# Optimization experiments

Measured on AMD Instinct MI355X. Metric: run time of the kernel, lower is better.

## Reference

```python
import jax, jax.numpy as jnp
import numpy as np

B = 16384          # batch
N = 24             # num_features / fields
CARD = 10000       # vocab per feature (all equal)
D = 16             # factor_dim
NI = N * (N - 1) // 2  # 276 pairwise interactions
H1, H2 = 128, 64


def setup_inputs() -> dict:
    key = jax.random.key(0)
    ks = jax.random.split(key, 10)
    x = jax.random.randint(ks[0], (B, N), 0, CARD, dtype=jnp.int32)
    # field-aware embedding table: E[f, id, field, :] is feature f's embedding w.r.t. field
    E = jax.random.normal(ks[1], (N, CARD, N, D), dtype=jnp.float32) * 0.01
    Wlin = jax.random.normal(ks[2], (N, CARD), dtype=jnp.float32) * 0.01
    blin = jnp.zeros((1,), dtype=jnp.float32)
    W1 = jax.random.normal(ks[3], (NI, H1), dtype=jnp.float32) * (1.0 / np.sqrt(NI))
    b1 = jnp.zeros((H1,), dtype=jnp.float32)
    W2 = jax.random.normal(ks[4], (H1, H2), dtype=jnp.float32) * (1.0 / np.sqrt(H1))
    b2 = jnp.zeros((H2,), dtype=jnp.float32)
    W3 = jax.random.normal(ks[5], (H2, 1), dtype=jnp.float32) * (1.0 / np.sqrt(H2))
    b3 = jnp.zeros((1,), dtype=jnp.float32)
    return {"x": x, "E": E, "Wlin": Wlin, "blin": blin,
            "W1": W1, "b1": b1, "W2": W2, "b2": b2, "W3": W3, "b3": b3}


def reference(x, E, Wlin, blin, W1, b1, W2, b2, W3, b3):
    feat_idx = jnp.arange(N)[None, :]              # [1, N]
    # factors[b, i, j, :] = embedding of feature i (value x[b,i]) w.r.t. field j
    factors = E[feat_idx, x]                        # [B, N, N, D]
    # interactions[b, i, j] = <factors[b,i,j], factors[b,j,i]>
    inter = jnp.sum(factors * jnp.swapaxes(factors, 1, 2), axis=-1)  # [B, N, N]
    iu, ju = jnp.triu_indices(N, k=1)
    pairs = inter[:, iu, ju]                        # [B, NI] strict upper triangle, row-major
    # FCN (dropout inactive at inference): relu -> relu -> linear
    h = jax.nn.relu(pairs @ W1 + b1)
    h = jax.nn.relu(h @ W2 + b2)
    nn_out = h @ W3 + b3                            # [B, 1]
    lin_out = jnp.sum(Wlin[feat_idx, x], axis=1, keepdims=True) + blin  # [B, 1]
    return lin_out + nn_out
```

## Files before the change

kernel.cpp:

```cpp
#include <hip/hip_runtime.h>

#define BB    16384
#define NF    24
#define CARDN 10000
#define DD    16
#define NI    276
#define H1N   128
#define H2N   64
#define SB    16
#define PSTR  17
#define HSTR  17

__global__ __launch_bounds__(256, 4) void fanfm_fused_kernel(
    const int* __restrict__ x, const float* __restrict__ E,
    const float* __restrict__ Wlin, const float* __restrict__ blin,
    const float* __restrict__ W1, const float* __restrict__ b1,
    const float* __restrict__ W2, const float* __restrict__ b2,
    const float* __restrict__ W3, const float* __restrict__ b3,
    float* __restrict__ out)
{
    __shared__ float pairsT[NI * PSTR];
    __shared__ float h1T[H1N * HSTR];
    __shared__ int   xs[SB * NF];
    __shared__ float lin_s[SB];
    __shared__ int   pi_tab[NI];
    __shared__ int   pj_tab[NI];

    float* h2T = pairsT;

    const int tid = threadIdx.x;
    const int b0  = blockIdx.x * SB;

    for (int idx = tid; idx < SB * NF; idx += 256) xs[idx] = x[b0 * NF + idx];
    for (int idx = tid; idx < NI; idx += 256) {
        int i = 0, rem = idx, cnt = NF - 1;
        while (rem >= cnt) { rem -= cnt; --cnt; ++i; }
        pi_tab[idx] = i;
        pj_tab[idx] = i + 1 + rem;
    }
    __syncthreads();

    if (tid < SB) {
        float l = blin[0] + b3[0];
        #pragma unroll
        for (int i = 0; i < NF; ++i) l += Wlin[i * CARDN + xs[tid * NF + i]];
        lin_s[tid] = l;
    }

    #pragma unroll 2
    for (int k = 0; k < (SB * NI + 255) / 256; ++k) {
        int idx = tid + k * 256;
        if (idx < SB * NI) {
            int s = idx / NI;
            int p = idx - s * NI;
            int i = pi_tab[p];
            int j = pj_tab[p];
            int xi = xs[s * NF + i];
            int xj = xs[s * NF + j];
            const float4* a = (const float4*)(E + ((size_t)i * CARDN + xi) * (NF * DD) + j * DD);
            const float4* c = (const float4*)(E + ((size_t)j * CARDN + xj) * (NF * DD) + i * DD);
            float4 a0 = a[0], a1 = a[1], a2 = a[2], a3 = a[3];
            float4 c0 = c[0], c1 = c[1], c2 = c[2], c3 = c[3];
            float d =
                a0.x*c0.x + a0.y*c0.y + a0.z*c0.z + a0.w*c0.w +
                a1.x*c1.x + a1.y*c1.y + a1.z*c1.z + a1.w*c1.w +
                a2.x*c2.x + a2.y*c2.y + a2.z*c2.z + a2.w*c2.w +
                a3.x*c3.x + a3.y*c3.y + a3.z*c3.z + a3.w*c3.w;
            pairsT[p * PSTR + s] = d;
        }
    }
    __syncthreads();

    {
        const int c4 = tid & 31;
        const int sg = tid >> 5;
        float acc[2][4] = {};
        #pragma unroll 4
        for (int p = 0; p < NI; ++p) {
            float4 w = *(const float4*)(W1 + p * H1N + c4 * 4);
            float pr0 = pairsT[p * PSTR + sg * 2 + 0];
            float pr1 = pairsT[p * PSTR + sg * 2 + 1];
            acc[0][0] = fmaf(pr0, w.x, acc[0][0]);
            acc[0][1] = fmaf(pr0, w.y, acc[0][1]);
            acc[0][2] = fmaf(pr0, w.z, acc[0][2]);
            acc[0][3] = fmaf(pr0, w.w, acc[0][3]);
            acc[1][0] = fmaf(pr1, w.x, acc[1][0]);
            acc[1][1] = fmaf(pr1, w.y, acc[1][1]);
            acc[1][2] = fmaf(pr1, w.z, acc[1][2]);
            acc[1][3] = fmaf(pr1, w.w, acc[1][3]);
        }
        float4 bb = *(const float4*)(b1 + c4 * 4);
        #pragma unroll
        for (int si = 0; si < 2; ++si) {
            int s = sg * 2 + si;
            h1T[(c4 * 4 + 0) * HSTR + s] = fmaxf(acc[si][0] + bb.x, 0.f);
            h1T[(c4 * 4 + 1) * HSTR + s] = fmaxf(acc[si][1] + bb.y, 0.f);
            h1T[(c4 * 4 + 2) * HSTR + s] = fmaxf(acc[si][2] + bb.z, 0.f);
            h1T[(c4 * 4 + 3) * HSTR + s] = fmaxf(acc[si][3] + bb.w, 0.f);
        }
    }
    __syncthreads();

    {
        const int c16 = tid & 15;
        const int sg2 = tid >> 4;
        float acc[4] = {};
        #pragma unroll 4
        for (int p = 0; p < H1N; ++p) {
            float4 w = *(const float4*)(W2 + p * H2N + c16 * 4);
            float pr = h1T[p * HSTR + sg2];
            acc[0] = fmaf(pr, w.x, acc[0]);
            acc[1] = fmaf(pr, w.y, acc[1]);
            acc[2] = fmaf(pr, w.z, acc[2]);
            acc[3] = fmaf(pr, w.w, acc[3]);
        }
        float4 bb = *(const float4*)(b2 + c16 * 4);
        h2T[(c16 * 4 + 0) * HSTR + sg2] = fmaxf(acc[0] + bb.x, 0.f);
        h2T[(c16 * 4 + 1) * HSTR + sg2] = fmaxf(acc[1] + bb.y, 0.f);
        h2T[(c16 * 4 + 2) * HSTR + sg2] = fmaxf(acc[2] + bb.z, 0.f);
        h2T[(c16 * 4 + 3) * HSTR + sg2] = fmaxf(acc[3] + bb.w, 0.f);
    }
    __syncthreads();

    {
        const int s  = tid >> 4;
        const int ko = tid & 15;
        float r = 0.f;
        #pragma unroll
        for (int kk = 0; kk < 4; ++kk) {
            int k = ko * 4 + kk;
            r = fmaf(h2T[k * HSTR + s], W3[k], r);
        }
        r += __shfl_xor(r, 1);
        r += __shfl_xor(r, 2);
        r += __shfl_xor(r, 4);
        r += __shfl_xor(r, 8);
        if (ko == 0) out[b0 + s] = r + lin_s[s];
    }
}

extern "C" void kernel_launch(void* const* d_in, const int* in_sizes, int n_in,
                              void* d_out, int out_size, void* d_ws, size_t ws_size,
                              hipStream_t stream) {
    const int*   x    = (const int*)  d_in[0];
    const float* E    = (const float*)d_in[1];
    const float* Wlin = (const float*)d_in[2];
    const float* blin = (const float*)d_in[3];
    const float* W1   = (const float*)d_in[4];
    const float* b1   = (const float*)d_in[5];
    const float* W2   = (const float*)d_in[6];
    const float* b2   = (const float*)d_in[7];
    const float* W3   = (const float*)d_in[8];
    const float* b3   = (const float*)d_in[9];
    float* out = (float*)d_out;

    fanfm_fused_kernel<<<BB / SB, 256, 0, stream>>>(
        x, E, Wlin, blin, W1, b1, W2, b2, W3, b3, out);
}
```

Baseline: 133.5 us.

## Specialize waves into embedding-gather producers and an MLP consumer wave

Halves samples per block to 8 and doubles the block to 512 threads. 448 threads gather the field-aware embeddings and compute the pairwise dot products. One 64-thread wave computes the linear term, then spins on an LDS atomic counter and runs all three MLP layers in registers, with a shuffle reduction at the end. This removes several block-wide barriers and the h2 staging buffer, and aims to overlap one block's MLP with other blocks' memory-bound gathers. In exchange a single wave does the whole MLP per block, and the tighter launch bound may limit registers.

```diff
diff --git a/kernel.cpp b/kernel.cpp
--- a/kernel.cpp
+++ b/kernel.cpp
@@ -7,11 +7,13 @@
 #define NI    276
 #define H1N   128
 #define H2N   64
-#define SB    16
-#define PSTR  17
-#define HSTR  17
+#define SB    8
+#define PSTR  9
+#define HSTR  9
+#define NPROD 448
+#define NPAIR (SB * NI)
 
-__global__ __launch_bounds__(256, 4) void fanfm_fused_kernel(
+__global__ __launch_bounds__(512, 8) void fanfm_pc_kernel(
     const int* __restrict__ x, const float* __restrict__ E,
     const float* __restrict__ Wlin, const float* __restrict__ blin,
     const float* __restrict__ W1, const float* __restrict__ b1,
@@ -22,120 +24,118 @@
     __shared__ float pairsT[NI * PSTR];
     __shared__ float h1T[H1N * HSTR];
     __shared__ int   xs[SB * NF];
-    __shared__ float lin_s[SB];
     __shared__ int   pi_tab[NI];
     __shared__ int   pj_tab[NI];
-
-    float* h2T = pairsT;
+    __shared__ int   done;
 
     const int tid = threadIdx.x;
     const int b0  = blockIdx.x * SB;
 
-    for (int idx = tid; idx < SB * NF; idx += 256) xs[idx] = x[b0 * NF + idx];
-    for (int idx = tid; idx < NI; idx += 256) {
-        int i = 0, rem = idx, cnt = NF - 1;
+    if (tid == 0) done = 0;
+    for (int idx = tid; idx < SB * NF; idx += 512) xs[idx] = x[b0 * NF + idx];
+    if (tid < NI) {
+        int i = 0, rem = tid, cnt = NF - 1;
         while (rem >= cnt) { rem -= cnt; --cnt; ++i; }
-        pi_tab[idx] = i;
-        pj_tab[idx] = i + 1 + rem;
+        pi_tab[tid] = i;
+        pj_tab[tid] = i + 1 + rem;
     }
     __syncthreads();
 
-    if (tid < SB) {
-        float l = blin[0] + b3[0];
+    if (tid < NPROD) {
+        #pragma unroll 2
+        for (int k = 0; k < 5; ++k) {
+            int idx = tid + k * NPROD;
+            if (idx < NPAIR) {
+                int s = idx / NI;
+                int p = idx - s * NI;
+                int i = pi_tab[p];
+                int j = pj_tab[p];
+                int xi = xs[s * NF + i];
+                int xj = xs[s * NF + j];
+                const float4* a = (const float4*)(E + ((size_t)i * CARDN + xi) * (NF * DD) + j * DD);
+                const float4* c = (const float4*)(E + ((size_t)j * CARDN + xj) * (NF * DD) + i * DD);
+                float4 a0 = a[0], a1 = a[1], a2 = a[2], a3 = a[3];
+                float4 c0 = c[0], c1 = c[1], c2 = c[2], c3 = c[3];
+                float d =
+                    a0.x*c0.x + a0.y*c0.y + a0.z*c0.z + a0.w*c0.w +
+                    a1.x*c1.x + a1.y*c1.y + a1.z*c1.z + a1.w*c1.w +
+                    a2.x*c2.x + a2.y*c2.y + a2.z*c2.z + a2.w*c2.w +
+                    a3.x*c3.x + a3.y*c3.y + a3.z*c3.z + a3.w*c3.w;
+                pairsT[p * PSTR + s] = d;
+            }
+        }
+        __threadfence_block();
+        atomicAdd(&done, 1);
+    } else {
+        const int ct = tid - NPROD;
+        const int s  = ct >> 3;
+        const int cg = ct & 7;
+
+        float lpart = 0.f;
         #pragma unroll
-        for (int i = 0; i < NF; ++i) l += Wlin[i * CARDN + xs[tid * NF + i]];
-        lin_s[tid] = l;
-    }
+        for (int f = cg * 3; f < cg * 3 + 3; ++f)
+            lpart += Wlin[f * CARDN + xs[s * NF + f]];
 
-    #pragma unroll 2
-    for (int k = 0; k < (SB * NI + 255) / 256; ++k) {
-        int idx = tid + k * 256;
-        if (idx < SB * NI) {
-            int s = idx / NI;
-            int p = idx - s * NI;
-            int i = pi_tab[p];
-            int j = pj_tab[p];
-            int xi = xs[s * NF + i];
-            int xj = xs[s * NF + j];
-            const float4* a = (const float4*)(E + ((size_t)i * CARDN + xi) * (NF * DD) + j * DD);
-            const float4* c = (const float4*)(E + ((size_t)j * CARDN + xj) * (NF * DD) + i * DD);
-            float4 a0 = a[0], a1 = a[1], a2 = a[2], a3 = a[3];
-            float4 c0 = c[0], c1 = c[1], c2 = c[2], c3 = c[3];
-            float d =
-                a0.x*c0.x + a0.y*c0.y + a0.z*c0.z + a0.w*c0.w +
-                a1.x*c1.x + a1.y*c1.y + a1.z*c1.z + a1.w*c1.w +
-                a2.x*c2.x + a2.y*c2.y + a2.z*c2.z + a2.w*c2.w +
-                a3.x*c3.x + a3.y*c3.y + a3.z*c3.z + a3.w*c3.w;
-            pairsT[p * PSTR + s] = d;
+        while (atomicAdd(&done, 0) < NPROD) __builtin_amdgcn_s_sleep(2);
+
+        float acc[16];
+        #pragma unroll
+        for (int c = 0; c < 16; ++c) acc[c] = 0.f;
+        for (int p = 0; p < NI; ++p) {
+            float pr = pairsT[p * PSTR + s];
+            const float4* wr = (const float4*)(W1 + p * H1N + cg * 16);
+            float4 w0 = wr[0], w1 = wr[1], w2 = wr[2], w3 = wr[3];
+            acc[0]  = fmaf(pr, w0.x, acc[0]);  acc[1]  = fmaf(pr, w0.y, acc[1]);
+            acc[2]  = fmaf(pr, w0.z, acc[2]);  acc[3]  = fmaf(pr, w0.w, acc[3]);
+            acc[4]  = fmaf(pr, w1.x, acc[4]);  acc[5]  = fmaf(pr, w1.y, acc[5]);
+            acc[6]  = fmaf(pr, w1.z, acc[6]);  acc[7]  = fmaf(pr, w1.w, acc[7]);
+            acc[8]  = fmaf(pr, w2.x, acc[8]);  acc[9]  = fmaf(pr, w2.y, acc[9]);
+            acc[10] = fmaf(pr, w2.z, acc[10]); acc[11] = fmaf(pr, w2.w, acc[11]);
+            acc[12] = fmaf(pr, w3.x, acc[12]); acc[13] = fmaf(pr, w3.y, acc[13]);
+            acc[14] = fmaf(pr, w3.z, acc[14]); acc[15] = fmaf(pr, w3.w, acc[15]);
         }
-    }
-    __syncthreads();
+        {
+            const float4* br = (const float4*)(b1 + cg * 16);
+            float4 bb0 = br[0], bb1 = br[1], bb2 = br[2], bb3 = br[3];
+            const float bbv[16] = {bb0.x,bb0.y,bb0.z,bb0.w, bb1.x,bb1.y,bb1.z,bb1.w,
+                                   bb2.x,bb2.y,bb2.z,bb2.w, bb3.x,bb3.y,bb3.z,bb3.w};
+            #pragma unroll
+            for (int c = 0; c < 16; ++c)
+                h1T[(cg * 16 + c) * HSTR + s] = fmaxf(acc[c] + bbv[c], 0.f);
+        }
 
-    {
-        const int c4 = tid & 31;
-        const int sg = tid >> 5;
-        float acc[2][4] = {};
-        #pragma unroll 4
-        for (int p = 0; p < NI; ++p) {
-            float4 w = *(const float4*)(W1 + p * H1N + c4 * 4);
-            float pr0 = pairsT[p * PSTR + sg * 2 + 0];
-            float pr1 = pairsT[p * PSTR + sg * 2 + 1];
-            acc[0][0] = fmaf(pr0, w.x, acc[0][0]);
-            acc[0][1] = fmaf(pr0, w.y, acc[0][1]);
-            acc[0][2] = fmaf(pr0, w.z, acc[0][2]);
-            acc[0][3] = fmaf(pr0, w.w, acc[0][3]);
-            acc[1][0] = fmaf(pr1, w.x, acc[1][0]);
-            acc[1][1] = fmaf(pr1, w.y, acc[1][1]);
-            acc[1][2] = fmaf(pr1, w.z, acc[1][2]);
-            acc[1][3] = fmaf(pr1, w.w, acc[1][3]);
+        float acc2[8];
+        #pragma unroll
+        for (int c = 0; c < 8; ++c) acc2[c] = 0.f;
+        for (int p = 0; p < H1N; ++p) {
+            float pr = h1T[p * HSTR + s];
+            const float4* wr = (const float4*)(W2 + p * H2N + cg * 8);
+            float4 w0 = wr[0], w1 = wr[1];
+            acc2[0] = fmaf(pr, w0.x, acc2[0]); acc2[1] = fmaf(pr, w0.y, acc2[1]);
+            acc2[2] = fmaf(pr, w0.z, acc2[2]); acc2[3] = fmaf(pr, w0.w, acc2[3]);
+            acc2[4] = fmaf(pr, w1.x, acc2[4]); acc2[5] = fmaf(pr, w1.y, acc2[5]);
+            acc2[6] = fmaf(pr, w1.z, acc2[6]); acc2[7] = fmaf(pr, w1.w, acc2[7]);
         }
-        float4 bb = *(const float4*)(b1 + c4 * 4);
-        #pragma unroll
-        for (int si = 0; si < 2; ++si) {
-            int s = sg * 2 + si;
-            h1T[(c4 * 4 + 0) * HSTR + s] = fmaxf(acc[si][0] + bb.x, 0.f);
-            h1T[(c4 * 4 + 1) * HSTR + s] = fmaxf(acc[si][1] + bb.y, 0.f);
-            h1T[(c4 * 4 + 2) * HSTR + s] = fmaxf(acc[si][2] + bb.z, 0.f);
-            h1T[(c4 * 4 + 3) * HSTR + s] = fmaxf(acc[si][3] + bb.w, 0.f);
-        }
-    }
-    __syncthreads();
 
-    {
-        const int c16 = tid & 15;
-        const int sg2 = tid >> 4;
-        float acc[4] = {};
-        #pragma unroll 4
-        for (int p = 0; p < H1N; ++p) {
-            float4 w = *(const float4*)(W2 + p * H2N + c16 * 4);
-            float pr = h1T[p * HSTR + sg2];
-            acc[0] = fmaf(pr, w.x, acc[0]);
-            acc[1] = fmaf(pr, w.y, acc[1]);
-            acc[2] = fmaf(pr, w.z, acc[2]);
-            acc[3] = fmaf(pr, w.w, acc[3]);
-        }
-        float4 bb = *(const float4*)(b2 + c16 * 4);
-        h2T[(c16 * 4 + 0) * HSTR + sg2] = fmaxf(acc[0] + bb.x, 0.f);
-        h2T[(c16 * 4 + 1) * HSTR + sg2] = fmaxf(acc[1] + bb.y, 0.f);
-        h2T[(c16 * 4 + 2) * HSTR + sg2] = fmaxf(acc[2] + bb.z, 0.f);
-        h2T[(c16 * 4 + 3) * HSTR + sg2] = fmaxf(acc[3] + bb.w, 0.f);
-    }
-    __syncthreads();
-
-    {
-        const int s  = tid >> 4;
-        const int ko = tid & 15;
-        float r = 0.f;
-        #pragma unroll
-        for (int kk = 0; kk < 4; ++kk) {
-            int k = ko * 4 + kk;
-            r = fmaf(h2T[k * HSTR + s], W3[k], r);
+        float r = lpart;
+        {
+            const float4* br = (const float4*)(b2 + cg * 8);
+            const float4* wr = (const float4*)(W3 + cg * 8);
+            float4 bb0 = br[0], bb1 = br[1];
+            float4 w30 = wr[0], w31 = wr[1];
+            r += fmaxf(acc2[0] + bb0.x, 0.f) * w30.x;
+            r += fmaxf(acc2[1] + bb0.y, 0.f) * w30.y;
+            r += fmaxf(acc2[2] + bb0.z, 0.f) * w30.z;
+            r += fmaxf(acc2[3] + bb0.w, 0.f) * w30.w;
+            r += fmaxf(acc2[4] + bb1.x, 0.f) * w31.x;
+            r += fmaxf(acc2[5] + bb1.y, 0.f) * w31.y;
+            r += fmaxf(acc2[6] + bb1.z, 0.f) * w31.z;
+            r += fmaxf(acc2[7] + bb1.w, 0.f) * w31.w;
         }
         r += __shfl_xor(r, 1);
         r += __shfl_xor(r, 2);
         r += __shfl_xor(r, 4);
-        r += __shfl_xor(r, 8);
-        if (ko == 0) out[b0 + s] = r + lin_s[s];
+        if (cg == 0) out[b0 + s] = r + blin[0] + b3[0];
     }
 }
 
@@ -154,6 +154,6 @@
     const float* b3   = (const float*)d_in[9];
     float* out = (float*)d_out;
 
-    fanfm_fused_kernel<<<BB / SB, 256, 0, stream>>>(
+    fanfm_pc_kernel<<<BB / SB, 512, 0, stream>>>(
         x, E, Wlin, blin, W1, b1, W2, b2, W3, b3, out);
 }
```

Result: slower. 236.8 us (+77.3%).

## Pipeline embedding row gathers into LDS with triple-buffered async loads

Applied to the files above, without the earlier changes.

Replaces per-thread scattered float4 gathers of embedding slices with async global_load_lds copies of each sample's 12-feature row group (all field slices of each feature) into a triple-buffered LDS ring. Dot products for pairs are computed from LDS one stage behind the loads, ordered by a pair table sorted by segment. The per-block sample count drops from 16 to 4, giving 4x more blocks, with 2 blocks per CU, and the MLP layers are remapped to 64 columns by 4 samples, with the second and third layers fused through a wave-wide shuffle reduction. The intent is to overlap gather latency with compute and coalesce the row reads, at the cost of more LDS, lower occupancy and a barrier every stage.

```diff
diff --git a/kernel.cpp b/kernel.cpp
--- a/kernel.cpp
+++ b/kernel.cpp
@@ -7,11 +7,22 @@
 #define NI    276
 #define H1N   128
 #define H2N   64
-#define SB    16
-#define PSTR  17
-#define HSTR  17
+#define SB    4
+#define PSTR  5
+#define GRP   12
+#define ROWF  368
+#define GF    (GRP * ROWF)
+#define F4PG  1104
 
-__global__ __launch_bounds__(256, 4) void fanfm_fused_kernel(
+
+__device__ __forceinline__ void gll16(const float* g, float* l) {
+    __builtin_amdgcn_global_load_lds(
+        (const __attribute__((address_space(1))) unsigned int*)(g),
+        (__attribute__((address_space(3))) unsigned int*)(l),
+        16, 0, 0);
+}
+
+__global__ __launch_bounds__(256, 2) void fanfm_pipe_kernel(
     const int* __restrict__ x, const float* __restrict__ E,
     const float* __restrict__ Wlin, const float* __restrict__ blin,
     const float* __restrict__ W1, const float* __restrict__ b1,
@@ -19,123 +30,116 @@
     const float* __restrict__ W3, const float* __restrict__ b3,
     float* __restrict__ out)
 {
+    __shared__ float buf[3 * GF];
     __shared__ float pairsT[NI * PSTR];
-    __shared__ float h1T[H1N * HSTR];
+    __shared__ float h1T[H1N * PSTR];
     __shared__ int   xs[SB * NF];
+    __shared__ int   ptab[NI];
     __shared__ float lin_s[SB];
-    __shared__ int   pi_tab[NI];
-    __shared__ int   pj_tab[NI];
-
-    float* h2T = pairsT;
+    __shared__ int   cnt01[2];
 
     const int tid = threadIdx.x;
     const int b0  = blockIdx.x * SB;
+    const int wb  = tid & ~63;
 
-    for (int idx = tid; idx < SB * NF; idx += 256) xs[idx] = x[b0 * NF + idx];
-    for (int idx = tid; idx < NI; idx += 256) {
-        int i = 0, rem = idx, cnt = NF - 1;
+    if (tid < SB * NF) xs[tid] = x[b0 * NF + tid];
+    if (tid < 2) cnt01[tid] = (tid == 0) ? 0 : 66;
+    __syncthreads();
+
+    for (int pp = tid; pp < NI; pp += 256) {
+        int i = 0, rem = pp, cnt = NF - 1;
         while (rem >= cnt) { rem -= cnt; --cnt; ++i; }
-        pi_tab[idx] = i;
-        pj_tab[idx] = i + 1 + rem;
+        int j = i + 1 + rem;
+        int seg = (j < GRP) ? 0 : 1;
+        int slot = atomicAdd(&cnt01[seg], 1);
+        ptab[slot] = i | (j << 5) | (pp << 10);
     }
     __syncthreads();
 
     if (tid < SB) {
         float l = blin[0] + b3[0];
         #pragma unroll
-        for (int i = 0; i < NF; ++i) l += Wlin[i * CARDN + xs[tid * NF + i]];
+        for (int f = 0; f < NF; ++f) l += Wlin[f * CARDN + xs[tid * NF + f]];
         lin_s[tid] = l;
     }
 
-    #pragma unroll 2
-    for (int k = 0; k < (SB * NI + 255) / 256; ++k) {
-        int idx = tid + k * 256;
-        if (idx < SB * NI) {
-            int s = idx / NI;
-            int p = idx - s * NI;
-            int i = pi_tab[p];
-            int j = pj_tab[p];
-            int xi = xs[s * NF + i];
-            int xj = xs[s * NF + j];
-            const float4* a = (const float4*)(E + ((size_t)i * CARDN + xi) * (NF * DD) + j * DD);
-            const float4* c = (const float4*)(E + ((size_t)j * CARDN + xj) * (NF * DD) + i * DD);
-            float4 a0 = a[0], a1 = a[1], a2 = a[2], a3 = a[3];
-            float4 c0 = c[0], c1 = c[1], c2 = c[2], c3 = c[3];
-            float d =
-                a0.x*c0.x + a0.y*c0.y + a0.z*c0.z + a0.w*c0.w +
-                a1.x*c1.x + a1.y*c1.y + a1.z*c1.z + a1.w*c1.w +
-                a2.x*c2.x + a2.y*c2.y + a2.z*c2.z + a2.w*c2.w +
-                a3.x*c3.x + a3.y*c3.y + a3.z*c3.z + a3.w*c3.w;
-            pairsT[p * PSTR + s] = d;
+    for (int t = 0; t <= 2 * SB; ++t) {
+        if (t < 2 * SB) {
+            const int g = t & 1;
+            const int s = t >> 1;
+            float* bt = buf + (t % 3) * GF;
+            #pragma unroll
+            for (int k = 0; k < 5; ++k) {
+                int idx = k * 256 + tid;
+                if (idx < F4PG) {
+                    int r   = idx / 92;
+                    int f4i = idx - r * 92;
+                    int c   = f4i >> 2;
+                    int q   = f4i & 3;
+                    int rg  = g * GRP + r;
+                    int j   = c + (c >= rg ? 1 : 0);
+                    const float* src = E
+                        + ((size_t)rg * CARDN + xs[s * NF + rg]) * (NF * DD)
+                        + j * DD + q * 4;
+                    gll16(src, bt + (k * 256 + wb) * 4);
+                }
+            }
         }
+        if (t >= 1) {
+            int segb, segn, s, bA, bB;
+            if (t & 1) { s = t >> 1;       segb = 0;  segn = 66;
+                         bA = (t - 1) % 3; bB = bA; }
+            else       { s = (t >> 1) - 1; segb = 66; segn = 210;
+                         bA = (t - 2) % 3; bB = (t - 1) % 3; }
+            if (tid < segn) {
+                int e = ptab[segb + tid];
+                int i = e & 31, j = (e >> 5) & 31, p = e >> 10;
+                const float4* ra = (const float4*)(buf
+                    + (i < GRP ? bA : bB) * GF + (i % GRP) * ROWF + (j - 1) * DD);
+                const float4* rc = (const float4*)(buf
+                    + (j < GRP ? bA : bB) * GF + (j % GRP) * ROWF + i * DD);
+                float4 a0 = ra[0], a1 = ra[1], a2 = ra[2], a3 = ra[3];
+                float4 c0 = rc[0], c1 = rc[1], c2 = rc[2], c3 = rc[3];
+                float d =
+                    a0.x*c0.x + a0.y*c0.y + a0.z*c0.z + a0.w*c0.w +
+                    a1.x*c1.x + a1.y*c1.y + a1.z*c1.z + a1.w*c1.w +
+                    a2.x*c2.x + a2.y*c2.y + a2.z*c2.z + a2.w*c2.w +
+                    a3.x*c3.x + a3.y*c3.y + a3.z*c3.z + a3.w*c3.w;
+                pairsT[p * PSTR + s] = d;
+            }
+        }
+        __syncthreads();
+    }
+
+    const int c2 = tid & 63;
+    const int sM = tid >> 6;
+    {
+        float a0 = 0.f, a1 = 0.f;
+        #pragma unroll 4
+        for (int p = 0; p < NI; ++p) {
+            float pr = pairsT[p * PSTR + sM];
+            float2 w = *(const float2*)(W1 + p * H1N + c2 * 2);
+            a0 = fmaf(pr, w.x, a0);
+            a1 = fmaf(pr, w.y, a1);
+        }
+        h1T[(c2 * 2 + 0) * PSTR + sM] = fmaxf(a0 + b1[c2 * 2 + 0], 0.f);
+        h1T[(c2 * 2 + 1) * PSTR + sM] = fmaxf(a1 + b1[c2 * 2 + 1], 0.f);
     }
     __syncthreads();
 
     {
-        const int c4 = tid & 31;
-        const int sg = tid >> 5;
-        float acc[2][4] = {};
+        float acc = 0.f;
         #pragma unroll 4
-        for (int p = 0; p < NI; ++p) {
-            float4 w = *(const float4*)(W1 + p * H1N + c4 * 4);
-            float pr0 = pairsT[p * PSTR + sg * 2 + 0];
-            float pr1 = pairsT[p * PSTR + sg * 2 + 1];
-            acc[0][0] = fmaf(pr0, w.x, acc[0][0]);
-            acc[0][1] = fmaf(pr0, w.y, acc[0][1]);
-            acc[0][2] = fmaf(pr0, w.z, acc[0][2]);
-            acc[0][3] = fmaf(pr0, w.w, acc[0][3]);
-            acc[1][0] = fmaf(pr1, w.x, acc[1][0]);
-            acc[1][1] = fmaf(pr1, w.y, acc[1][1]);
-            acc[1][2] = fmaf(pr1, w.z, acc[1][2]);
-            acc[1][3] = fmaf(pr1, w.w, acc[1][3]);
-        }
-        float4 bb = *(const float4*)(b1 + c4 * 4);
-        #pragma unroll
-        for (int si = 0; si < 2; ++si) {
-            int s = sg * 2 + si;
-            h1T[(c4 * 4 + 0) * HSTR + s] = fmaxf(acc[si][0] + bb.x, 0.f);
-            h1T[(c4 * 4 + 1) * HSTR + s] = fmaxf(acc[si][1] + bb.y, 0.f);
-            h1T[(c4 * 4 + 2) * HSTR + s] = fmaxf(acc[si][2] + bb.z, 0.f);
-            h1T[(c4 * 4 + 3) * HSTR + s] = fmaxf(acc[si][3] + bb.w, 0.f);
-        }
-    }
-    __syncthreads();
-
-    {
-        const int c16 = tid & 15;
-        const int sg2 = tid >> 4;
-        float acc[4] = {};
-        #pragma unroll 4
-        for (int p = 0; p < H1N; ++p) {
-            float4 w = *(const float4*)(W2 + p * H2N + c16 * 4);
-            float pr = h1T[p * HSTR + sg2];
-            acc[0] = fmaf(pr, w.x, acc[0]);
-            acc[1] = fmaf(pr, w.y, acc[1]);
-            acc[2] = fmaf(pr, w.z, acc[2]);
-            acc[3] = fmaf(pr, w.w, acc[3]);
-        }
-        float4 bb = *(const float4*)(b2 + c16 * 4);
-        h2T[(c16 * 4 + 0) * HSTR + sg2] = fmaxf(acc[0] + bb.x, 0.f);
-        h2T[(c16 * 4 + 1) * HSTR + sg2] = fmaxf(acc[1] + bb.y, 0.f);
-        h2T[(c16 * 4 + 2) * HSTR + sg2] = fmaxf(acc[2] + bb.z, 0.f);
-        h2T[(c16 * 4 + 3) * HSTR + sg2] = fmaxf(acc[3] + bb.w, 0.f);
-    }
-    __syncthreads();
-
-    {
-        const int s  = tid >> 4;
-        const int ko = tid & 15;
-        float r = 0.f;
-        #pragma unroll
-        for (int kk = 0; kk < 4; ++kk) {
-            int k = ko * 4 + kk;
-            r = fmaf(h2T[k * HSTR + s], W3[k], r);
-        }
+        for (int p = 0; p < H1N; ++p)
+            acc = fmaf(h1T[p * PSTR + sM], W2[p * H2N + c2], acc);
+        float r = fmaxf(acc + b2[c2], 0.f) * W3[c2];
         r += __shfl_xor(r, 1);
         r += __shfl_xor(r, 2);
         r += __shfl_xor(r, 4);
         r += __shfl_xor(r, 8);
-        if (ko == 0) out[b0 + s] = r + lin_s[s];
+        r += __shfl_xor(r, 16);
+        r += __shfl_xor(r, 32);
+        if (c2 == 0) out[b0 + sM] = r + lin_s[sM];
     }
 }
 
@@ -153,7 +157,8 @@
     const float* W3   = (const float*)d_in[8];
     const float* b3   = (const float*)d_in[9];
     float* out = (float*)d_out;
+    (void)d_ws; (void)ws_size; (void)in_sizes; (void)n_in; (void)out_size;
 
-    fanfm_fused_kernel<<<BB / SB, 256, 0, stream>>>(
+    fanfm_pipe_kernel<<<BB / SB, 256, 0, stream>>>(
         x, E, Wlin, blin, W1, b1, W2, b2, W3, b3, out);
 }
```

Result: slower. 320.2 us (+139.8%).

## Stage full embedding rows in LDS with double-buffered per-sample gathers

Applied to the files above, without the earlier changes.

Each sample's 24 field-aware embedding rows are loaded contiguously into a double-buffered shared-memory tile. The next sample's rows are prefetched while pairwise dot products for the current sample are computed from LDS. The second and third MLP layers are also fused into a single reduction. This targets scattered 64-byte global gathers, but it uses about 120 KB of LDS per block and needs a sync each sample, which limits the CU to one block.

```diff
diff --git a/kernel.cpp b/kernel.cpp
--- a/kernel.cpp
+++ b/kernel.cpp
@@ -1,17 +1,20 @@
 #include <hip/hip_runtime.h>
 
-#define BB    16384
-#define NF    24
-#define CARDN 10000
-#define DD    16
-#define NI    276
-#define H1N   128
-#define H2N   64
-#define SB    16
-#define PSTR  17
-#define HSTR  17
+#define BB     16384
+#define NF     24
+#define CARDN  10000
+#define DD     16
+#define NI     276
+#define H1N    128
+#define H2N    64
+#define SB     16
+#define NT     576
+#define CH_F4  5
+#define ROW_F4 121
+#define BUF_F4 (NF * ROW_F4)
+#define PSTR   17
 
-__global__ __launch_bounds__(256, 4) void fanfm_fused_kernel(
+__global__ __launch_bounds__(NT, 1) void fanfm_r8_kernel(
     const int* __restrict__ x, const float* __restrict__ E,
     const float* __restrict__ Wlin, const float* __restrict__ blin,
     const float* __restrict__ W1, const float* __restrict__ b1,
@@ -19,123 +22,122 @@
     const float* __restrict__ W3, const float* __restrict__ b3,
     float* __restrict__ out)
 {
-    __shared__ float pairsT[NI * PSTR];
-    __shared__ float h1T[H1N * HSTR];
-    __shared__ int   xs[SB * NF];
-    __shared__ float lin_s[SB];
-    __shared__ int   pi_tab[NI];
-    __shared__ int   pj_tab[NI];
-
-    float* h2T = pairsT;
+    __shared__ float4 buf[2 * BUF_F4];
+    __shared__ float  pairsT[NI * PSTR];
+    __shared__ float  h1T[H1N * PSTR];
+    __shared__ int    xs[SB * NF];
+    __shared__ float  lin_s[SB];
 
     const int tid = threadIdx.x;
     const int b0  = blockIdx.x * SB;
 
-    for (int idx = tid; idx < SB * NF; idx += 256) xs[idx] = x[b0 * NF + idx];
-    for (int idx = tid; idx < NI; idx += 256) {
-        int i = 0, rem = idx, cnt = NF - 1;
-        while (rem >= cnt) { rem -= cnt; --cnt; ++i; }
-        pi_tab[idx] = i;
-        pj_tab[idx] = i + 1 + rem;
-    }
+    if (tid < SB * NF) xs[tid] = x[b0 * NF + tid];
     __syncthreads();
 
     if (tid < SB) {
         float l = blin[0] + b3[0];
         #pragma unroll
-        for (int i = 0; i < NF; ++i) l += Wlin[i * CARDN + xs[tid * NF + i]];
+        for (int f = 0; f < NF; ++f) l += Wlin[f * CARDN + xs[tid * NF + f]];
         lin_s[tid] = l;
     }
 
-    #pragma unroll 2
-    for (int k = 0; k < (SB * NI + 255) / 256; ++k) {
-        int idx = tid + k * 256;
-        if (idx < SB * NI) {
-            int s = idx / NI;
-            int p = idx - s * NI;
-            int i = pi_tab[p];
-            int j = pj_tab[p];
-            int xi = xs[s * NF + i];
-            int xj = xs[s * NF + j];
-            const float4* a = (const float4*)(E + ((size_t)i * CARDN + xi) * (NF * DD) + j * DD);
-            const float4* c = (const float4*)(E + ((size_t)j * CARDN + xj) * (NF * DD) + i * DD);
-            float4 a0 = a[0], a1 = a[1], a2 = a[2], a3 = a[3];
-            float4 c0 = c[0], c1 = c[1], c2 = c[2], c3 = c[3];
+    int pi = 0, pj = 0;
+    if (tid < NI) {
+        int rem = tid, cnt = NF - 1;
+        while (rem >= cnt) { rem -= cnt; --cnt; ++pi; }
+        pj = pi + 1 + rem;
+    }
+
+    float4 st[4];
+
+    #pragma unroll
+    for (int k = 0; k < 4; ++k) {
+        int v = tid + k * NT;
+        int r = v / 96, w = v - r * 96;
+        st[k] = *((const float4*)(E + ((size_t)r * CARDN + xs[r]) * (NF * DD)) + w);
+    }
+    #pragma unroll
+    for (int k = 0; k < 4; ++k) {
+        int v = tid + k * NT;
+        int r = v / 96, w = v - r * 96;
+        int c = w >> 2, q = w & 3;
+        buf[r * ROW_F4 + c * CH_F4 + q] = st[k];
+    }
+    __syncthreads();
+
+    for (int t = 0; t < SB; ++t) {
+        if (t + 1 < SB) {
+            #pragma unroll
+            for (int k = 0; k < 4; ++k) {
+                int v = tid + k * NT;
+                int r = v / 96, w = v - r * 96;
+                st[k] = *((const float4*)(E +
+                    ((size_t)r * CARDN + xs[(t + 1) * NF + r]) * (NF * DD)) + w);
+            }
+        }
+        if (tid < NI) {
+            const float4* A = &buf[(t & 1) * BUF_F4 + pi * ROW_F4 + pj * CH_F4];
+            const float4* C = &buf[(t & 1) * BUF_F4 + pj * ROW_F4 + pi * CH_F4];
+            float4 a0 = A[0], a1 = A[1], a2 = A[2], a3 = A[3];
+            float4 c0 = C[0], c1 = C[1], c2 = C[2], c3 = C[3];
             float d =
                 a0.x*c0.x + a0.y*c0.y + a0.z*c0.z + a0.w*c0.w +
                 a1.x*c1.x + a1.y*c1.y + a1.z*c1.z + a1.w*c1.w +
                 a2.x*c2.x + a2.y*c2.y + a2.z*c2.z + a2.w*c2.w +
                 a3.x*c3.x + a3.y*c3.y + a3.z*c3.z + a3.w*c3.w;
-            pairsT[p * PSTR + s] = d;
+            pairsT[tid * PSTR + t] = d;
         }
+        if (t + 1 < SB) {
+            #pragma unroll
+            for (int k = 0; k < 4; ++k) {
+                int v = tid + k * NT;
+                int r = v / 96, w = v - r * 96;
+                int c = w >> 2, q = w & 3;
+                buf[((t + 1) & 1) * BUF_F4 + r * ROW_F4 + c * CH_F4 + q] = st[k];
+            }
+        }
+        __syncthreads();
     }
-    __syncthreads();
 
-    {
+    if (tid < 512) {
         const int c4 = tid & 31;
-        const int sg = tid >> 5;
-        float acc[2][4] = {};
+        const int s  = tid >> 5;
+        float acc[4] = {};
         #pragma unroll 4
         for (int p = 0; p < NI; ++p) {
+            float pr = pairsT[p * PSTR + s];
             float4 w = *(const float4*)(W1 + p * H1N + c4 * 4);
-            float pr0 = pairsT[p * PSTR + sg * 2 + 0];
-            float pr1 = pairsT[p * PSTR + sg * 2 + 1];
-            acc[0][0] = fmaf(pr0, w.x, acc[0][0]);
-            acc[0][1] = fmaf(pr0, w.y, acc[0][1]);
-            acc[0][2] = fmaf(pr0, w.z, acc[0][2]);
-            acc[0][3] = fmaf(pr0, w.w, acc[0][3]);
-            acc[1][0] = fmaf(pr1, w.x, acc[1][0]);
-            acc[1][1] = fmaf(pr1, w.y, acc[1][1]);
-            acc[1][2] = fmaf(pr1, w.z, acc[1][2]);
-            acc[1][3] = fmaf(pr1, w.w, acc[1][3]);
-        }
-        float4 bb = *(const float4*)(b1 + c4 * 4);
-        #pragma unroll
-        for (int si = 0; si < 2; ++si) {
-            int s = sg * 2 + si;
-            h1T[(c4 * 4 + 0) * HSTR + s] = fmaxf(acc[si][0] + bb.x, 0.f);
-            h1T[(c4 * 4 + 1) * HSTR + s] = fmaxf(acc[si][1] + bb.y, 0.f);
-            h1T[(c4 * 4 + 2) * HSTR + s] = fmaxf(acc[si][2] + bb.z, 0.f);
-            h1T[(c4 * 4 + 3) * HSTR + s] = fmaxf(acc[si][3] + bb.w, 0.f);
-        }
-    }
-    __syncthreads();
-
-    {
-        const int c16 = tid & 15;
-        const int sg2 = tid >> 4;
-        float acc[4] = {};
-        #pragma unroll 4
-        for (int p = 0; p < H1N; ++p) {
-            float4 w = *(const float4*)(W2 + p * H2N + c16 * 4);
-            float pr = h1T[p * HSTR + sg2];
             acc[0] = fmaf(pr, w.x, acc[0]);
             acc[1] = fmaf(pr, w.y, acc[1]);
             acc[2] = fmaf(pr, w.z, acc[2]);
             acc[3] = fmaf(pr, w.w, acc[3]);
         }
-        float4 bb = *(const float4*)(b2 + c16 * 4);
-        h2T[(c16 * 4 + 0) * HSTR + sg2] = fmaxf(acc[0] + bb.x, 0.f);
-        h2T[(c16 * 4 + 1) * HSTR + sg2] = fmaxf(acc[1] + bb.y, 0.f);
-        h2T[(c16 * 4 + 2) * HSTR + sg2] = fmaxf(acc[2] + bb.z, 0.f);
-        h2T[(c16 * 4 + 3) * HSTR + sg2] = fmaxf(acc[3] + bb.w, 0.f);
+        float4 bb = *(const float4*)(b1 + c4 * 4);
+        h1T[(c4 * 4 + 0) * PSTR + s] = fmaxf(acc[0] + bb.x, 0.f);
+        h1T[(c4 * 4 + 1) * PSTR + s] = fmaxf(acc[1] + bb.y, 0.f);
+        h1T[(c4 * 4 + 2) * PSTR + s] = fmaxf(acc[2] + bb.z, 0.f);
+        h1T[(c4 * 4 + 3) * PSTR + s] = fmaxf(acc[3] + bb.w, 0.f);
     }
     __syncthreads();
 
-    {
-        const int s  = tid >> 4;
-        const int ko = tid & 15;
-        float r = 0.f;
-        #pragma unroll
-        for (int kk = 0; kk < 4; ++kk) {
-            int k = ko * 4 + kk;
-            r = fmaf(h2T[k * HSTR + s], W3[k], r);
+    if (tid < 512) {
+        const int cl = tid & 31;
+        const int s  = tid >> 5;
+        float a0 = 0.f, a1 = 0.f;
+        #pragma unroll 4
+        for (int p = 0; p < H1N; ++p) {
+            float pr = h1T[p * PSTR + s];
+            a0 = fmaf(pr, W2[p * H2N + cl], a0);
+            a1 = fmaf(pr, W2[p * H2N + cl + 32], a1);
         }
+        float r = fmaxf(a0 + b2[cl],      0.f) * W3[cl]
+                + fmaxf(a1 + b2[cl + 32], 0.f) * W3[cl + 32];
         r += __shfl_xor(r, 1);
         r += __shfl_xor(r, 2);
         r += __shfl_xor(r, 4);
         r += __shfl_xor(r, 8);
-        if (ko == 0) out[b0 + s] = r + lin_s[s];
+        r += __shfl_xor(r, 16);
+        if (cl == 0) out[b0 + s] = r + lin_s[s];
     }
 }
 
@@ -153,7 +155,8 @@
     const float* W3   = (const float*)d_in[8];
     const float* b3   = (const float*)d_in[9];
     float* out = (float*)d_out;
+    (void)d_ws; (void)ws_size; (void)in_sizes; (void)n_in; (void)out_size;
 
-    fanfm_fused_kernel<<<BB / SB, 256, 0, stream>>>(
+    fanfm_r8_kernel<<<BB / SB, NT, 0, stream>>>(
         x, E, Wlin, blin, W1, b1, W2, b2, W3, b3, out);
 }
```

New measurement: 202.1 us. 1.51x slower.
